# Kernel optimization log

Measured on AMD Instinct MI355X. Metric: run time of the kernel, lower is better.

## Reference

```python
import jax, jax.numpy as jnp
import numpy as np

B, S, H, D = 16, 2048, 768, 128
ATTR_MAX, ITEMS_MAX = 8, 32  # static equivalents of attr_type_ids.max() / item_position_ids max (data generated to hit these)


def setup_inputs() -> dict:
    key = jax.random.key(0)
    k1, k2, k3, k4 = jax.random.split(key, 4)
    return {
        "attention_mask": jnp.ones((B, S), dtype=jnp.int32),
        "hidden_states": jax.random.normal(k1, (B, S, H), dtype=jnp.float32),
        "attr_type_ids": jax.random.randint(k2, (B, S), 0, ATTR_MAX + 1),
        "item_position_ids": jax.random.randint(k3, (B, S), 0, ITEMS_MAX + 1),
        "W": jax.random.normal(k4, (H, D), dtype=jnp.float32) * (1.0 / np.sqrt(H)),
        "b": jnp.zeros((D,), dtype=jnp.float32),
    }


def reference(attention_mask, hidden_states, attr_type_ids, item_position_ids, W, b):
    # linear projection: [B,S,H] @ [H,D] -> [B,S,D]
    h = jnp.einsum('bsh,hd->bsd', hidden_states, W) + b
    Bn, Sn, Dn = h.shape

    # segmented mean over (attr_id, item_id) groups; attr/item id 0 (and >max, e.g. the 50 pad sentinel) are invalid
    valid = (attr_type_ids >= 1) & (attr_type_ids <= ATTR_MAX) & \
            (item_position_ids >= 1) & (item_position_ids <= ITEMS_MAX)
    batch_idx = jnp.arange(Bn)[:, None]
    seg = (batch_idx * ATTR_MAX + (attr_type_ids - 1)) * ITEMS_MAX + (item_position_ids - 1)
    nseg = Bn * ATTR_MAX * ITEMS_MAX
    seg = jnp.where(valid, seg, nseg)  # dump invalid tokens into extra segment
    flat_seg = seg.reshape(-1)

    sums = jax.ops.segment_sum(h.reshape(-1, Dn), flat_seg, num_segments=nseg + 1)[:nseg]
    counts = jax.ops.segment_sum(valid.reshape(-1).astype(h.dtype), flat_seg, num_segments=nseg + 1)[:nseg]

    sums = sums.reshape(Bn, ATTR_MAX, ITEMS_MAX, Dn)
    counts = counts.reshape(Bn, ATTR_MAX, ITEMS_MAX)
    empty = counts == 0
    pooled = sums / jnp.where(empty, jnp.ones_like(counts), counts)[..., None]
    return pooled, empty, h
```

## Files before the change

kernel.cpp:

```cpp
#include <hip/hip_runtime.h>
#include <hip/hip_bf16.h>

#define Bn 16
#define Sn 2048
#define Hn 768
#define Dn 128
#define AT 8
#define IT 32
#define NSEG (Bn*AT*IT)

typedef __attribute__((ext_vector_type(4))) float f32x4;
typedef __attribute__((ext_vector_type(4))) int   i32x4;
typedef __attribute__((ext_vector_type(8))) short bf16x8;
typedef __attribute__((ext_vector_type(4))) short s16x4;

__device__ __forceinline__ unsigned short f2bf(float f){
  union { float f; unsigned u; } v; v.f = f;
  unsigned r = v.u + 0x7FFFu + ((v.u >> 16) & 1u);
  return (unsigned short)(r >> 16);
}

__global__ __launch_bounds__(256) void k_prep(const float* __restrict__ W,
                                              unsigned short* __restrict__ Wt){
  __shared__ float sT[64][65];
  const int tid = threadIdx.x;
  const int k0 = (blockIdx.x % 12) * 64;
  const int d0 = (blockIdx.x / 12) * 64;
  const int rr = tid >> 4;
  const int cg = tid & 15;

  #pragma unroll
  for (int p = 0; p < 4; ++p){
    int k = rr + p*16;
    f32x4 v = *(const f32x4*)&W[(size_t)(k0 + k)*Dn + d0 + cg*4];
    sT[k][cg*4+0] = v[0]; sT[k][cg*4+1] = v[1];
    sT[k][cg*4+2] = v[2]; sT[k][cg*4+3] = v[3];
  }
  __syncthreads();
  #pragma unroll
  for (int p = 0; p < 4; ++p){
    int d = rr + p*16;
    s16x4 t;
    #pragma unroll
    for (int j = 0; j < 4; ++j) t[j] = (short)f2bf(sT[cg*4+j][d]);
    *(s16x4*)&Wt[(size_t)(d0 + d)*Hn + k0 + cg*4] = t;
  }
}

__global__ __launch_bounds__(256) void k_gemm(const float* __restrict__ X,
        const unsigned short* __restrict__ Wt, const float* __restrict__ bias,
        float* __restrict__ Hout){
  __shared__ unsigned char sA[2][64*128];
  __shared__ unsigned char sB[2][128*128];
  const int tid  = threadIdx.x;
  const int lane = tid & 63;
  const int wave = tid >> 6;
  const int m0 = blockIdx.x * 64;

  const int ar = tid >> 2, akq = tid & 3;
  const int bc = tid >> 1, bkh = tid & 1;
  const float*          Ap = X  + (size_t)(m0 + ar)*Hn + akq*4;
  const unsigned short* Bp = Wt + (size_t)bc*Hn + bkh*32;

  int aw[4], bw[4];
  #pragma unroll
  for (int c=0;c<4;c++) aw[c] = ar*128 + ((akq*8 + c*32) ^ ((ar&7)<<4));
  #pragma unroll
  for (int c=0;c<4;c++) bw[c] = bc*128 + ((bkh*64 + c*16) ^ ((bc&7)<<4));

  int abase[4], aswz[4];
  #pragma unroll
  for (int mi=0;mi<4;mi++){
    int row = mi*16 + (lane&15);
    abase[mi] = row*128; aswz[mi] = (row&7)<<4;
  }
  int bbase[2], bswz[2];
  #pragma unroll
  for (int ni=0;ni<2;ni++){
    int col = wave*32 + ni*16 + (lane&15);
    bbase[ni] = col*128; bswz[ni] = (col&7)<<4;
  }
  const int kblk = (lane>>4)*16;

  f32x4 acc[4][2];
  #pragma unroll
  for (int mi=0;mi<4;mi++)
    #pragma unroll
    for (int ni=0;ni<2;ni++) acc[mi][ni] = (f32x4){0.f,0.f,0.f,0.f};

  f32x4 av[4]; i32x4 bv[4];
  #pragma unroll
  for (int c=0;c<4;c++) av[c] = *(const f32x4*)(Ap + c*16);
  #pragma unroll
  for (int c=0;c<4;c++) bv[c] = *(const i32x4*)(Bp + c*8);
  #pragma unroll
  for (int c=0;c<4;c++){
    s16x4 t;
    t[0]=(short)f2bf(av[c][0]); t[1]=(short)f2bf(av[c][1]);
    t[2]=(short)f2bf(av[c][2]); t[3]=(short)f2bf(av[c][3]);
    *(s16x4*)&sA[0][aw[c]] = t;
  }
  #pragma unroll
  for (int c=0;c<4;c++) *(i32x4*)&sB[0][bw[c]] = bv[c];
  __syncthreads();

  int cur = 0;
  for (int step=0; step<12; ++step){
    if (step < 11){
      #pragma unroll
      for (int c=0;c<4;c++) av[c] = *(const f32x4*)(Ap + (step+1)*64 + c*16);
      #pragma unroll
      for (int c=0;c<4;c++) bv[c] = *(const i32x4*)(Bp + (step+1)*64 + c*8);
    }
    #pragma unroll
    for (int ks=0; ks<2; ++ks){
      bf16x8 af[4], bfv[2];
      #pragma unroll
      for (int mi=0;mi<4;mi++)
        af[mi] = *(const bf16x8*)&sA[cur][abase[mi] + ((ks*64 + kblk) ^ aswz[mi])];
      #pragma unroll
      for (int ni=0;ni<2;ni++)
        bfv[ni] = *(const bf16x8*)&sB[cur][bbase[ni] + ((ks*64 + kblk) ^ bswz[ni])];
      #pragma unroll
      for (int mi=0;mi<4;mi++)
        #pragma unroll
        for (int ni=0;ni<2;ni++)
          acc[mi][ni] = __builtin_amdgcn_mfma_f32_16x16x32_bf16(af[mi], bfv[ni], acc[mi][ni], 0, 0, 0);
    }
    if (step < 11){
      #pragma unroll
      for (int c=0;c<4;c++){
        s16x4 t;
        t[0]=(short)f2bf(av[c][0]); t[1]=(short)f2bf(av[c][1]);
        t[2]=(short)f2bf(av[c][2]); t[3]=(short)f2bf(av[c][3]);
        *(s16x4*)&sA[cur^1][aw[c]] = t;
      }
      #pragma unroll
      for (int c=0;c<4;c++) *(i32x4*)&sB[cur^1][bw[c]] = bv[c];
    }
    __syncthreads();
    cur ^= 1;
  }

  #pragma unroll
  for (int ni=0;ni<2;ni++){
    int col = wave*32 + ni*16 + (lane&15);
    float bb = bias[col];
    #pragma unroll
    for (int mi=0;mi<4;mi++){
      int row0 = m0 + mi*16 + (lane>>4)*4;
      #pragma unroll
      for (int r=0;r<4;r++)
        Hout[(size_t)(row0 + r)*Dn + col] = acc[mi][ni][r] + bb;
    }
  }
}

__global__ __launch_bounds__(256) void k_scan(const int* __restrict__ attr,
        const int* __restrict__ item, const float* __restrict__ Hsrc,
        float* __restrict__ pooled, float* __restrict__ empty){
  __shared__ float ssum[4][IT][64];
  __shared__ int   slist[4][512];
  __shared__ int   scnt[IT];

  const int wg  = blockIdx.x;
  const int dh  = wg & 1;
  const int a   = (wg >> 1) & 7;
  const int b   = wg >> 4;
  const int tid = threadIdx.x;
  const int wv  = tid >> 6;
  const int lane = tid & 63;

  #pragma unroll
  for (int i = 0; i < IT; ++i) ssum[wv][i][lane] = 0.f;
  if (tid < IT) scnt[tid] = 0;

  const int tok0 = wv * 512;
  const int gbase = b * Sn;
  int nm = 0;
  #pragma unroll
  for (int g = 0; g < 8; ++g){
    int tok = tok0 + g*64 + lane;
    int avv = attr[gbase + tok], ivv = item[gbase + tok];
    bool m = (avv == a+1) && (ivv >= 1) && (ivv <= IT);
    unsigned long long mask = __ballot(m);
    int pos = nm + __popcll(mask & ((1ull << lane) - 1ull));
    if (m) slist[wv][pos] = ((ivv-1) << 16) | tok;
    nm += __popcll(mask);
  }
  __syncthreads();

  for (int e = lane; e < nm; e += 64) atomicAdd(&scnt[slist[wv][e] >> 16], 1);

  const float* hb = Hsrc + (size_t)b*Sn*Dn + dh*64 + lane;
  int e = 0;
  for (; e + 8 <= nm; e += 8){
    int idx[8]; float v[8];
    #pragma unroll
    for (int j=0;j<8;j++) idx[j] = slist[wv][e+j];
    #pragma unroll
    for (int j=0;j<8;j++) v[j] = hb[(size_t)(idx[j] & 0xffff)*Dn];
    #pragma unroll
    for (int j=0;j<8;j++) ssum[wv][idx[j]>>16][lane] += v[j];
  }
  for (; e < nm; ++e){
    int idx = slist[wv][e];
    ssum[wv][idx>>16][lane] += hb[(size_t)(idx & 0xffff)*Dn];
  }
  __syncthreads();

  float* outp = pooled + (size_t)(b*AT + a)*IT*Dn + dh*64;
  for (int o = tid; o < IT*64; o += 256){
    int i = o >> 6, d = o & 63;
    float s = ssum[0][i][d] + ssum[1][i][d] + ssum[2][i][d] + ssum[3][i][d];
    int cnt = scnt[i];
    outp[i*Dn + d] = s / (float)(cnt > 0 ? cnt : 1);
  }
  if (dh == 0 && tid < IT)
    empty[(b*AT + a)*IT + tid] = (scnt[tid] == 0) ? 1.f : 0.f;
}

extern "C" void kernel_launch(void* const* d_in, const int* in_sizes, int n_in,
                              void* d_out, int out_size, void* d_ws, size_t ws_size,
                              hipStream_t stream) {
  const float* hidden = (const float*)d_in[1];
  const int*   attr   = (const int*)  d_in[2];
  const int*   item   = (const int*)  d_in[3];
  const float* W      = (const float*)d_in[4];
  const float* bias   = (const float*)d_in[5];

  float* pooled = (float*)d_out;
  float* empty  = pooled + (size_t)NSEG*Dn;
  float* Hout   = empty  + NSEG;

  unsigned short* Wt = (unsigned short*)d_ws;

  k_prep<<<24, 256, 0, stream>>>(W, Wt);
  k_gemm<<<(Bn*Sn)/64, 256, 0, stream>>>(hidden, Wt, bias, Hout);
  k_scan<<<Bn*AT*2, 256, 0, stream>>>(attr, item, Hout, pooled, empty);
}
```

Measured before the change: 39.43 us.

## Deepen GEMM global prefetch to two stages with register double-buffering

The GEMM main loop now keeps two sets of register buffers, so global loads are issued two K-steps ahead. The LDS store of the previously loaded tile is moved before the MFMA block, and the loop is fully unrolled with a compile-time buffer index. The float-to-bf16 conversion also switches to the HIP intrinsic. This aims to hide more global memory latency in a bandwidth-bound GEMM, at the cost of higher register pressure that may reduce occupancy.

```diff
diff --git a/kernel.cpp b/kernel.cpp
--- a/kernel.cpp
+++ b/kernel.cpp
@@ -15,9 +15,8 @@
 typedef __attribute__((ext_vector_type(4))) short s16x4;
 
 __device__ __forceinline__ unsigned short f2bf(float f){
-  union { float f; unsigned u; } v; v.f = f;
-  unsigned r = v.u + 0x7FFFu + ((v.u >> 16) & 1u);
-  return (unsigned short)(r >> 16);
+  __hip_bfloat16 h = __float2bfloat16(f);
+  return *reinterpret_cast<unsigned short*>(&h);
 }
 
 __global__ __launch_bounds__(256) void k_prep(const float* __restrict__ W,
@@ -88,29 +87,51 @@
     #pragma unroll
     for (int ni=0;ni<2;ni++) acc[mi][ni] = (f32x4){0.f,0.f,0.f,0.f};
 
-  f32x4 av[4]; i32x4 bv[4];
-  #pragma unroll
-  for (int c=0;c<4;c++) av[c] = *(const f32x4*)(Ap + c*16);
-  #pragma unroll
-  for (int c=0;c<4;c++) bv[c] = *(const i32x4*)(Bp + c*8);
+  f32x4 av[2][4]; i32x4 bv[2][4];
+
+  #pragma unroll
+  for (int c=0;c<4;c++) av[0][c] = *(const f32x4*)(Ap + c*16);
+  #pragma unroll
+  for (int c=0;c<4;c++) bv[0][c] = *(const i32x4*)(Bp + c*8);
   #pragma unroll
   for (int c=0;c<4;c++){
     s16x4 t;
-    t[0]=(short)f2bf(av[c][0]); t[1]=(short)f2bf(av[c][1]);
-    t[2]=(short)f2bf(av[c][2]); t[3]=(short)f2bf(av[c][3]);
+    t[0]=(short)f2bf(av[0][c][0]); t[1]=(short)f2bf(av[0][c][1]);
+    t[2]=(short)f2bf(av[0][c][2]); t[3]=(short)f2bf(av[0][c][3]);
     *(s16x4*)&sA[0][aw[c]] = t;
   }
   #pragma unroll
-  for (int c=0;c<4;c++) *(i32x4*)&sB[0][bw[c]] = bv[c];
-  __syncthreads();
-
-  int cur = 0;
+  for (int c=0;c<4;c++) *(i32x4*)&sB[0][bw[c]] = bv[0][c];
+  #pragma unroll
+  for (int c=0;c<4;c++) av[1][c] = *(const f32x4*)(Ap + 64 + c*16);
+  #pragma unroll
+  for (int c=0;c<4;c++) bv[1][c] = *(const i32x4*)(Bp + 64 + c*8);
+  #pragma unroll
+  for (int c=0;c<4;c++) av[0][c] = *(const f32x4*)(Ap + 128 + c*16);
+  #pragma unroll
+  for (int c=0;c<4;c++) bv[0][c] = *(const i32x4*)(Bp + 128 + c*8);
+  __syncthreads();
+
+  #pragma unroll
   for (int step=0; step<12; ++step){
+    const int cur = step & 1;
+    const int p   = (step+1) & 1;
     if (step < 11){
       #pragma unroll
-      for (int c=0;c<4;c++) av[c] = *(const f32x4*)(Ap + (step+1)*64 + c*16);
-      #pragma unroll
-      for (int c=0;c<4;c++) bv[c] = *(const i32x4*)(Bp + (step+1)*64 + c*8);
+      for (int c=0;c<4;c++){
+        s16x4 t;
+        t[0]=(short)f2bf(av[p][c][0]); t[1]=(short)f2bf(av[p][c][1]);
+        t[2]=(short)f2bf(av[p][c][2]); t[3]=(short)f2bf(av[p][c][3]);
+        *(s16x4*)&sA[cur^1][aw[c]] = t;
+      }
+      #pragma unroll
+      for (int c=0;c<4;c++) *(i32x4*)&sB[cur^1][bw[c]] = bv[p][c];
+    }
+    if (step < 9){
+      #pragma unroll
+      for (int c=0;c<4;c++) av[p][c] = *(const f32x4*)(Ap + (step+3)*64 + c*16);
+      #pragma unroll
+      for (int c=0;c<4;c++) bv[p][c] = *(const i32x4*)(Bp + (step+3)*64 + c*8);
     }
     #pragma unroll
     for (int ks=0; ks<2; ++ks){
@@ -127,19 +148,7 @@
         for (int ni=0;ni<2;ni++)
           acc[mi][ni] = __builtin_amdgcn_mfma_f32_16x16x32_bf16(af[mi], bfv[ni], acc[mi][ni], 0, 0, 0);
     }
-    if (step < 11){
-      #pragma unroll
-      for (int c=0;c<4;c++){
-        s16x4 t;
-        t[0]=(short)f2bf(av[c][0]); t[1]=(short)f2bf(av[c][1]);
-        t[2]=(short)f2bf(av[c][2]); t[3]=(short)f2bf(av[c][3]);
-        *(s16x4*)&sA[cur^1][aw[c]] = t;
-      }
-      #pragma unroll
-      for (int c=0;c<4;c++) *(i32x4*)&sB[cur^1][bw[c]] = bv[c];
-    }
     __syncthreads();
-    cur ^= 1;
   }
 
   #pragma unroll
```

Result: no change. 39.84 us (+1.0%).

## Fuse GEMM and segmented-mean scan into one kernel with per-batch completion flags

Applied to the files above, without the earlier changes.

Merges the projection GEMM and the segment-pooling scan into a single kernel. The first 256 tiles go on to do the scan work after their GEMM tile, reusing the shared memory through a union. Each scan block waits on a per-batch atomic counter until all 32 GEMM tiles for that batch have written their H rows. The change removes one kernel launch and the gap between launches, and lets the scan for early batches overlap with GEMM tiles still running. In exchange it relies on inter-block spin-waiting, which could deadlock if the waiting blocks occupy the GPU before the producing tiles are scheduled, and it swaps the manual bf16 rounding for the library conversion.

```diff
diff --git a/kernel.cpp b/kernel.cpp
--- a/kernel.cpp
+++ b/kernel.cpp
@@ -15,15 +15,17 @@
 typedef __attribute__((ext_vector_type(4))) short s16x4;
 
 __device__ __forceinline__ unsigned short f2bf(float f){
-  union { float f; unsigned u; } v; v.f = f;
-  unsigned r = v.u + 0x7FFFu + ((v.u >> 16) & 1u);
-  return (unsigned short)(r >> 16);
+  __hip_bfloat16 h = __float2bfloat16(f);
+  return *reinterpret_cast<unsigned short*>(&h);
 }
 
 __global__ __launch_bounds__(256) void k_prep(const float* __restrict__ W,
-                                              unsigned short* __restrict__ Wt){
+                                              unsigned short* __restrict__ Wt,
+                                              int* __restrict__ flags){
   __shared__ float sT[64][65];
   const int tid = threadIdx.x;
+  if (blockIdx.x == 0 && tid < Bn)
+    __hip_atomic_store(&flags[tid], 0, __ATOMIC_RELAXED, __HIP_MEMORY_SCOPE_AGENT);
   const int k0 = (blockIdx.x % 12) * 64;
   const int d0 = (blockIdx.x / 12) * 64;
   const int rr = tid >> 4;
@@ -47,133 +49,137 @@
   }
 }
 
-__global__ __launch_bounds__(256) void k_gemm(const float* __restrict__ X,
+__global__ __launch_bounds__(256) void k_fused(const float* __restrict__ X,
         const unsigned short* __restrict__ Wt, const float* __restrict__ bias,
-        float* __restrict__ Hout){
-  __shared__ unsigned char sA[2][64*128];
-  __shared__ unsigned char sB[2][128*128];
+        const int* __restrict__ attr, const int* __restrict__ item,
+        float* __restrict__ Hout, float* __restrict__ pooled,
+        float* __restrict__ empty, int* __restrict__ flags){
+  __shared__ union {
+    struct { unsigned char a[2][64*128]; unsigned char b[2][128*128]; } g;
+    struct { float ssum[4][IT][64]; int slist[4][512]; int scnt[IT]; } s;
+  } u;
+
   const int tid  = threadIdx.x;
   const int lane = tid & 63;
   const int wave = tid >> 6;
-  const int m0 = blockIdx.x * 64;
-
-  const int ar = tid >> 2, akq = tid & 3;
-  const int bc = tid >> 1, bkh = tid & 1;
-  const float*          Ap = X  + (size_t)(m0 + ar)*Hn + akq*4;
-  const unsigned short* Bp = Wt + (size_t)bc*Hn + bkh*32;
-
-  int aw[4], bw[4];
-  #pragma unroll
-  for (int c=0;c<4;c++) aw[c] = ar*128 + ((akq*8 + c*32) ^ ((ar&7)<<4));
-  #pragma unroll
-  for (int c=0;c<4;c++) bw[c] = bc*128 + ((bkh*64 + c*16) ^ ((bc&7)<<4));
-
-  int abase[4], aswz[4];
-  #pragma unroll
-  for (int mi=0;mi<4;mi++){
-    int row = mi*16 + (lane&15);
-    abase[mi] = row*128; aswz[mi] = (row&7)<<4;
-  }
-  int bbase[2], bswz[2];
-  #pragma unroll
-  for (int ni=0;ni<2;ni++){
-    int col = wave*32 + ni*16 + (lane&15);
-    bbase[ni] = col*128; bswz[ni] = (col&7)<<4;
-  }
-  const int kblk = (lane>>4)*16;
-
-  f32x4 acc[4][2];
-  #pragma unroll
-  for (int mi=0;mi<4;mi++)
-    #pragma unroll
-    for (int ni=0;ni<2;ni++) acc[mi][ni] = (f32x4){0.f,0.f,0.f,0.f};
-
-  f32x4 av[4]; i32x4 bv[4];
-  #pragma unroll
-  for (int c=0;c<4;c++) av[c] = *(const f32x4*)(Ap + c*16);
-  #pragma unroll
-  for (int c=0;c<4;c++) bv[c] = *(const i32x4*)(Bp + c*8);
-  #pragma unroll
-  for (int c=0;c<4;c++){
-    s16x4 t;
-    t[0]=(short)f2bf(av[c][0]); t[1]=(short)f2bf(av[c][1]);
-    t[2]=(short)f2bf(av[c][2]); t[3]=(short)f2bf(av[c][3]);
-    *(s16x4*)&sA[0][aw[c]] = t;
-  }
-  #pragma unroll
-  for (int c=0;c<4;c++) *(i32x4*)&sB[0][bw[c]] = bv[c];
-  __syncthreads();
-
-  int cur = 0;
-  for (int step=0; step<12; ++step){
-    if (step < 11){
+  const int tile = blockIdx.x;
+  const int m0 = tile * 64;
+
+  {
+    const int ar = tid >> 2, akq = tid & 3;
+    const int bc = tid >> 1, bkh = tid & 1;
+    const float*          Ap = X  + (size_t)(m0 + ar)*Hn + akq*4;
+    const unsigned short* Bp = Wt + (size_t)bc*Hn + bkh*32;
+
+    int aw[4], bw[4];
+    #pragma unroll
+    for (int c=0;c<4;c++) aw[c] = ar*128 + ((akq*8 + c*32) ^ ((ar&7)<<4));
+    #pragma unroll
+    for (int c=0;c<4;c++) bw[c] = bc*128 + ((bkh*64 + c*16) ^ ((bc&7)<<4));
+
+    int abase[4], aswz[4];
+    #pragma unroll
+    for (int mi=0;mi<4;mi++){
+      int row = mi*16 + (lane&15);
+      abase[mi] = row*128; aswz[mi] = (row&7)<<4;
+    }
+    int bbase[2], bswz[2];
+    #pragma unroll
+    for (int ni=0;ni<2;ni++){
+      int col = wave*32 + ni*16 + (lane&15);
+      bbase[ni] = col*128; bswz[ni] = (col&7)<<4;
+    }
+    const int kblk = (lane>>4)*16;
+
+    f32x4 acc[4][2];
+    #pragma unroll
+    for (int mi=0;mi<4;mi++)
       #pragma unroll
-      for (int c=0;c<4;c++) av[c] = *(const f32x4*)(Ap + (step+1)*64 + c*16);
+      for (int ni=0;ni<2;ni++) acc[mi][ni] = (f32x4){0.f,0.f,0.f,0.f};
+
+    f32x4 av[4]; i32x4 bv[4];
+    #pragma unroll
+    for (int c=0;c<4;c++) av[c] = *(const f32x4*)(Ap + c*16);
+    #pragma unroll
+    for (int c=0;c<4;c++) bv[c] = *(const i32x4*)(Bp + c*8);
+    #pragma unroll
+    for (int c=0;c<4;c++){
+      s16x4 t;
+      t[0]=(short)f2bf(av[c][0]); t[1]=(short)f2bf(av[c][1]);
+      t[2]=(short)f2bf(av[c][2]); t[3]=(short)f2bf(av[c][3]);
+      *(s16x4*)&u.g.a[0][aw[c]] = t;
+    }
+    #pragma unroll
+    for (int c=0;c<4;c++) *(i32x4*)&u.g.b[0][bw[c]] = bv[c];
+    __syncthreads();
+
+    int cur = 0;
+    for (int step=0; step<12; ++step){
+      if (step < 11){
+        #pragma unroll
+        for (int c=0;c<4;c++) av[c] = *(const f32x4*)(Ap + (step+1)*64 + c*16);
+        #pragma unroll
+        for (int c=0;c<4;c++) bv[c] = *(const i32x4*)(Bp + (step+1)*64 + c*8);
+      }
       #pragma unroll
-      for (int c=0;c<4;c++) bv[c] = *(const i32x4*)(Bp + (step+1)*64 + c*8);
-    }
-    #pragma unroll
-    for (int ks=0; ks<2; ++ks){
-      bf16x8 af[4], bfv[2];
+      for (int ks=0; ks<2; ++ks){
+        bf16x8 af[4], bfv[2];
+        #pragma unroll
+        for (int mi=0;mi<4;mi++)
+          af[mi] = *(const bf16x8*)&u.g.a[cur][abase[mi] + ((ks*64 + kblk) ^ aswz[mi])];
+        #pragma unroll
+        for (int ni=0;ni<2;ni++)
+          bfv[ni] = *(const bf16x8*)&u.g.b[cur][bbase[ni] + ((ks*64 + kblk) ^ bswz[ni])];
+        #pragma unroll
+        for (int mi=0;mi<4;mi++)
+          #pragma unroll
+          for (int ni=0;ni<2;ni++)
+            acc[mi][ni] = __builtin_amdgcn_mfma_f32_16x16x32_bf16(af[mi], bfv[ni], acc[mi][ni], 0, 0, 0);
+      }
+      if (step < 11){
+        #pragma unroll
+        for (int c=0;c<4;c++){
+          s16x4 t;
+          t[0]=(short)f2bf(av[c][0]); t[1]=(short)f2bf(av[c][1]);
+          t[2]=(short)f2bf(av[c][2]); t[3]=(short)f2bf(av[c][3]);
+          *(s16x4*)&u.g.a[cur^1][aw[c]] = t;
+        }
+        #pragma unroll
+        for (int c=0;c<4;c++) *(i32x4*)&u.g.b[cur^1][bw[c]] = bv[c];
+      }
+      __syncthreads();
+      cur ^= 1;
+    }
+
+    #pragma unroll
+    for (int ni=0;ni<2;ni++){
+      int col = wave*32 + ni*16 + (lane&15);
+      float bb = bias[col];
       #pragma unroll
-      for (int mi=0;mi<4;mi++)
-        af[mi] = *(const bf16x8*)&sA[cur][abase[mi] + ((ks*64 + kblk) ^ aswz[mi])];
-      #pragma unroll
-      for (int ni=0;ni<2;ni++)
-        bfv[ni] = *(const bf16x8*)&sB[cur][bbase[ni] + ((ks*64 + kblk) ^ bswz[ni])];
-      #pragma unroll
-      for (int mi=0;mi<4;mi++)
-        #pragma unroll
-        for (int ni=0;ni<2;ni++)
-          acc[mi][ni] = __builtin_amdgcn_mfma_f32_16x16x32_bf16(af[mi], bfv[ni], acc[mi][ni], 0, 0, 0);
-    }
-    if (step < 11){
-      #pragma unroll
-      for (int c=0;c<4;c++){
-        s16x4 t;
-        t[0]=(short)f2bf(av[c][0]); t[1]=(short)f2bf(av[c][1]);
-        t[2]=(short)f2bf(av[c][2]); t[3]=(short)f2bf(av[c][3]);
-        *(s16x4*)&sA[cur^1][aw[c]] = t;
-      }
-      #pragma unroll
-      for (int c=0;c<4;c++) *(i32x4*)&sB[cur^1][bw[c]] = bv[c];
-    }
-    __syncthreads();
-    cur ^= 1;
-  }
-
-  #pragma unroll
-  for (int ni=0;ni<2;ni++){
-    int col = wave*32 + ni*16 + (lane&15);
-    float bb = bias[col];
-    #pragma unroll
-    for (int mi=0;mi<4;mi++){
-      int row0 = m0 + mi*16 + (lane>>4)*4;
-      #pragma unroll
-      for (int r=0;r<4;r++)
-        Hout[(size_t)(row0 + r)*Dn + col] = acc[mi][ni][r] + bb;
-    }
-  }
-}
-
-__global__ __launch_bounds__(256) void k_scan(const int* __restrict__ attr,
-        const int* __restrict__ item, const float* __restrict__ Hsrc,
-        float* __restrict__ pooled, float* __restrict__ empty){
-  __shared__ float ssum[4][IT][64];
-  __shared__ int   slist[4][512];
-  __shared__ int   scnt[IT];
-
-  const int wg  = blockIdx.x;
+      for (int mi=0;mi<4;mi++){
+        int row0 = m0 + mi*16 + (lane>>4)*4;
+        #pragma unroll
+        for (int r=0;r<4;r++)
+          Hout[(size_t)(row0 + r)*Dn + col] = acc[mi][ni][r] + bb;
+      }
+    }
+  }
+
+  __syncthreads();
+  if (tid == 0)
+    __hip_atomic_fetch_add(&flags[tile >> 5], 1, __ATOMIC_RELEASE, __HIP_MEMORY_SCOPE_AGENT);
+
+  if (tile >= Bn*AT*2) return;
+
+  const int wg  = tile;
   const int dh  = wg & 1;
   const int a   = (wg >> 1) & 7;
   const int b   = wg >> 4;
-  const int tid = threadIdx.x;
-  const int wv  = tid >> 6;
-  const int lane = tid & 63;
-
-  #pragma unroll
-  for (int i = 0; i < IT; ++i) ssum[wv][i][lane] = 0.f;
-  if (tid < IT) scnt[tid] = 0;
+  const int wv  = wave;
+
+  #pragma unroll
+  for (int i = 0; i < IT; ++i) u.s.ssum[wv][i][lane] = 0.f;
+  if (tid < IT) u.s.scnt[tid] = 0;
 
   const int tok0 = wv * 512;
   const int gbase = b * Sn;
@@ -185,39 +191,46 @@
     bool m = (avv == a+1) && (ivv >= 1) && (ivv <= IT);
     unsigned long long mask = __ballot(m);
     int pos = nm + __popcll(mask & ((1ull << lane) - 1ull));
-    if (m) slist[wv][pos] = ((ivv-1) << 16) | tok;
+    if (m) u.s.slist[wv][pos] = ((ivv-1) << 16) | tok;
     nm += __popcll(mask);
   }
   __syncthreads();
 
-  for (int e = lane; e < nm; e += 64) atomicAdd(&scnt[slist[wv][e] >> 16], 1);
-
-  const float* hb = Hsrc + (size_t)b*Sn*Dn + dh*64 + lane;
+  for (int e = lane; e < nm; e += 64) atomicAdd(&u.s.scnt[u.s.slist[wv][e] >> 16], 1);
+
+  if (tid == 0){
+    while (__hip_atomic_load(&flags[b], __ATOMIC_ACQUIRE, __HIP_MEMORY_SCOPE_AGENT) < 32)
+      __builtin_amdgcn_s_sleep(2);
+  }
+  __syncthreads();
+  (void)__hip_atomic_load(&flags[b], __ATOMIC_ACQUIRE, __HIP_MEMORY_SCOPE_AGENT);
+
+  const float* hb = Hout + (size_t)b*Sn*Dn + dh*64 + lane;
   int e = 0;
   for (; e + 8 <= nm; e += 8){
     int idx[8]; float v[8];
     #pragma unroll
-    for (int j=0;j<8;j++) idx[j] = slist[wv][e+j];
+    for (int j=0;j<8;j++) idx[j] = u.s.slist[wv][e+j];
     #pragma unroll
     for (int j=0;j<8;j++) v[j] = hb[(size_t)(idx[j] & 0xffff)*Dn];
     #pragma unroll
-    for (int j=0;j<8;j++) ssum[wv][idx[j]>>16][lane] += v[j];
+    for (int j=0;j<8;j++) u.s.ssum[wv][idx[j]>>16][lane] += v[j];
   }
   for (; e < nm; ++e){
-    int idx = slist[wv][e];
-    ssum[wv][idx>>16][lane] += hb[(size_t)(idx & 0xffff)*Dn];
+    int idx = u.s.slist[wv][e];
+    u.s.ssum[wv][idx>>16][lane] += hb[(size_t)(idx & 0xffff)*Dn];
   }
   __syncthreads();
 
   float* outp = pooled + (size_t)(b*AT + a)*IT*Dn + dh*64;
   for (int o = tid; o < IT*64; o += 256){
     int i = o >> 6, d = o & 63;
-    float s = ssum[0][i][d] + ssum[1][i][d] + ssum[2][i][d] + ssum[3][i][d];
-    int cnt = scnt[i];
+    float s = u.s.ssum[0][i][d] + u.s.ssum[1][i][d] + u.s.ssum[2][i][d] + u.s.ssum[3][i][d];
+    int cnt = u.s.scnt[i];
     outp[i*Dn + d] = s / (float)(cnt > 0 ? cnt : 1);
   }
   if (dh == 0 && tid < IT)
-    empty[(b*AT + a)*IT + tid] = (scnt[tid] == 0) ? 1.f : 0.f;
+    empty[(b*AT + a)*IT + tid] = (u.s.scnt[tid] == 0) ? 1.f : 0.f;
 }
 
 extern "C" void kernel_launch(void* const* d_in, const int* in_sizes, int n_in,
@@ -234,8 +247,9 @@
   float* Hout   = empty  + NSEG;
 
   unsigned short* Wt = (unsigned short*)d_ws;
-
-  k_prep<<<24, 256, 0, stream>>>(W, Wt);
-  k_gemm<<<(Bn*Sn)/64, 256, 0, stream>>>(hidden, Wt, bias, Hout);
-  k_scan<<<Bn*AT*2, 256, 0, stream>>>(attr, item, Hout, pooled, empty);
-}
+  int* flags = (int*)((char*)d_ws + 196608);
+
+  k_prep<<<24, 256, 0, stream>>>(W, Wt, flags);
+  k_fused<<<(Bn*Sn)/64, 256, 0, stream>>>(hidden, Wt, bias, attr, item,
+                                          Hout, pooled, empty, flags);
+}
```

New measurement: 91.28 us. 2.32x slower.

## Load B fragments directly from global and deepen A prefetch pipeline

Applied to the files above, without the earlier changes.

The GEMM kernel stops staging the transposed bf16 weight tile in LDS and instead loads each wave's B fragments straight from global memory into registers, double-buffered across K steps. The A tile now uses a two-deep register prefetch, converting the next step's data into LDS before issuing loads for the step after, with raw s_barrier and sched_barrier in place of __syncthreads. The float-to-bf16 conversion also switches to the HIP intrinsic. This is meant to cut LDS traffic and capacity and to hide global load latency better, at the cost of more registers and redundant global reads of W across waves and blocks.

```diff
diff --git a/kernel.cpp b/kernel.cpp
--- a/kernel.cpp
+++ b/kernel.cpp
@@ -15,9 +15,8 @@
 typedef __attribute__((ext_vector_type(4))) short s16x4;
 
 __device__ __forceinline__ unsigned short f2bf(float f){
-  union { float f; unsigned u; } v; v.f = f;
-  unsigned r = v.u + 0x7FFFu + ((v.u >> 16) & 1u);
-  return (unsigned short)(r >> 16);
+  __hip_bfloat16 h = __float2bfloat16(f);
+  return *reinterpret_cast<unsigned short*>(&h);
 }
 
 __global__ __launch_bounds__(256) void k_prep(const float* __restrict__ W,
@@ -51,36 +50,34 @@
         const unsigned short* __restrict__ Wt, const float* __restrict__ bias,
         float* __restrict__ Hout){
   __shared__ unsigned char sA[2][64*128];
-  __shared__ unsigned char sB[2][128*128];
   const int tid  = threadIdx.x;
   const int lane = tid & 63;
   const int wave = tid >> 6;
-  const int m0 = blockIdx.x * 64;
-
-  const int ar = tid >> 2, akq = tid & 3;
-  const int bc = tid >> 1, bkh = tid & 1;
-  const float*          Ap = X  + (size_t)(m0 + ar)*Hn + akq*4;
-  const unsigned short* Bp = Wt + (size_t)bc*Hn + bkh*32;
-
-  int aw[4], bw[4];
-  #pragma unroll
-  for (int c=0;c<4;c++) aw[c] = ar*128 + ((akq*8 + c*32) ^ ((ar&7)<<4));
-  #pragma unroll
-  for (int c=0;c<4;c++) bw[c] = bc*128 + ((bkh*64 + c*16) ^ ((bc&7)<<4));
+  const int m0   = blockIdx.x * 64;
+  const int r16  = lane & 15, kg = lane >> 4;
+
+  const int r0 = tid >> 4;
+  const int kq = tid & 15;
+  const float* Ap = X + (size_t)(m0 + r0)*Hn + kq*4;
+  int awoff[4];
+  #pragma unroll
+  for (int i=0;i<4;i++){
+    int row = r0 + i*16;
+    awoff[i] = row*128 + ((kq*8) ^ ((row&7)<<4));
+  }
+
+  const unsigned short* Bp[2];
+  #pragma unroll
+  for (int ni=0;ni<2;ni++)
+    Bp[ni] = Wt + (size_t)(wave*32 + ni*16 + r16)*Hn + kg*8;
 
   int abase[4], aswz[4];
   #pragma unroll
   for (int mi=0;mi<4;mi++){
-    int row = mi*16 + (lane&15);
+    int row = mi*16 + r16;
     abase[mi] = row*128; aswz[mi] = (row&7)<<4;
   }
-  int bbase[2], bswz[2];
-  #pragma unroll
-  for (int ni=0;ni<2;ni++){
-    int col = wave*32 + ni*16 + (lane&15);
-    bbase[ni] = col*128; bswz[ni] = (col&7)<<4;
-  }
-  const int kblk = (lane>>4)*16;
+  const int kblk = kg*16;
 
   f32x4 acc[4][2];
   #pragma unroll
@@ -88,67 +85,79 @@
     #pragma unroll
     for (int ni=0;ni<2;ni++) acc[mi][ni] = (f32x4){0.f,0.f,0.f,0.f};
 
-  f32x4 av[4]; i32x4 bv[4];
-  #pragma unroll
-  for (int c=0;c<4;c++) av[c] = *(const f32x4*)(Ap + c*16);
-  #pragma unroll
-  for (int c=0;c<4;c++) bv[c] = *(const i32x4*)(Bp + c*8);
-  #pragma unroll
-  for (int c=0;c<4;c++){
+  f32x4  a4[2][4];
+  bf16x8 bv[2][4];
+
+  #pragma unroll
+  for (int i=0;i<4;i++) a4[0][i] = *(const f32x4*)(Ap + (size_t)i*16*Hn);
+  #pragma unroll
+  for (int i=0;i<4;i++) a4[1][i] = *(const f32x4*)(Ap + (size_t)i*16*Hn + 64);
+  #pragma unroll
+  for (int ks=0;ks<2;ks++)
+    #pragma unroll
+    for (int ni=0;ni<2;ni++)
+      bv[0][ks*2+ni] = *(const bf16x8*)(Bp[ni] + ks*32);
+  #pragma unroll
+  for (int i=0;i<4;i++){
     s16x4 t;
-    t[0]=(short)f2bf(av[c][0]); t[1]=(short)f2bf(av[c][1]);
-    t[2]=(short)f2bf(av[c][2]); t[3]=(short)f2bf(av[c][3]);
-    *(s16x4*)&sA[0][aw[c]] = t;
-  }
-  #pragma unroll
-  for (int c=0;c<4;c++) *(i32x4*)&sB[0][bw[c]] = bv[c];
-  __syncthreads();
-
-  int cur = 0;
-  for (int step=0; step<12; ++step){
-    if (step < 11){
-      #pragma unroll
-      for (int c=0;c<4;c++) av[c] = *(const f32x4*)(Ap + (step+1)*64 + c*16);
-      #pragma unroll
-      for (int c=0;c<4;c++) bv[c] = *(const i32x4*)(Bp + (step+1)*64 + c*8);
-    }
-    #pragma unroll
-    for (int ks=0; ks<2; ++ks){
-      bf16x8 af[4], bfv[2];
+    t[0]=(short)f2bf(a4[0][i][0]); t[1]=(short)f2bf(a4[0][i][1]);
+    t[2]=(short)f2bf(a4[0][i][2]); t[3]=(short)f2bf(a4[0][i][3]);
+    *(s16x4*)&sA[0][awoff[i]] = t;
+  }
+  asm volatile("s_waitcnt lgkmcnt(0)" ::: "memory");
+  __builtin_amdgcn_s_barrier();
+  __builtin_amdgcn_sched_barrier(0);
+
+  #pragma unroll
+  for (int s=0; s<12; ++s){
+    const int pb = (s+1)&1;
+    if (s < 11){
+      #pragma unroll
+      for (int i=0;i<4;i++){
+        s16x4 t;
+        t[0]=(short)f2bf(a4[pb][i][0]); t[1]=(short)f2bf(a4[pb][i][1]);
+        t[2]=(short)f2bf(a4[pb][i][2]); t[3]=(short)f2bf(a4[pb][i][3]);
+        *(s16x4*)&sA[pb][awoff[i]] = t;
+      }
+    }
+    if (s < 10){
+      #pragma unroll
+      for (int i=0;i<4;i++)
+        a4[s&1][i] = *(const f32x4*)(Ap + (size_t)i*16*Hn + (s+2)*64);
+    }
+    if (s < 11){
+      #pragma unroll
+      for (int ks=0;ks<2;ks++)
+        #pragma unroll
+        for (int ni=0;ni<2;ni++)
+          bv[pb][ks*2+ni] = *(const bf16x8*)(Bp[ni] + (s+1)*64 + ks*32);
+    }
+    #pragma unroll
+    for (int ks=0;ks<2;ks++){
+      bf16x8 af[4];
       #pragma unroll
       for (int mi=0;mi<4;mi++)
-        af[mi] = *(const bf16x8*)&sA[cur][abase[mi] + ((ks*64 + kblk) ^ aswz[mi])];
-      #pragma unroll
-      for (int ni=0;ni<2;ni++)
-        bfv[ni] = *(const bf16x8*)&sB[cur][bbase[ni] + ((ks*64 + kblk) ^ bswz[ni])];
+        af[mi] = *(const bf16x8*)&sA[s&1][abase[mi] + ((ks*64 + kblk) ^ aswz[mi])];
       #pragma unroll
       for (int mi=0;mi<4;mi++)
         #pragma unroll
         for (int ni=0;ni<2;ni++)
-          acc[mi][ni] = __builtin_amdgcn_mfma_f32_16x16x32_bf16(af[mi], bfv[ni], acc[mi][ni], 0, 0, 0);
-    }
-    if (step < 11){
-      #pragma unroll
-      for (int c=0;c<4;c++){
-        s16x4 t;
-        t[0]=(short)f2bf(av[c][0]); t[1]=(short)f2bf(av[c][1]);
-        t[2]=(short)f2bf(av[c][2]); t[3]=(short)f2bf(av[c][3]);
-        *(s16x4*)&sA[cur^1][aw[c]] = t;
-      }
-      #pragma unroll
-      for (int c=0;c<4;c++) *(i32x4*)&sB[cur^1][bw[c]] = bv[c];
-    }
-    __syncthreads();
-    cur ^= 1;
+          acc[mi][ni] = __builtin_amdgcn_mfma_f32_16x16x32_bf16(af[mi], bv[s&1][ks*2+ni], acc[mi][ni], 0, 0, 0);
+    }
+    if (s < 11){
+      asm volatile("s_waitcnt lgkmcnt(0)" ::: "memory");
+      __builtin_amdgcn_s_barrier();
+      __builtin_amdgcn_sched_barrier(0);
+    }
   }
 
   #pragma unroll
   for (int ni=0;ni<2;ni++){
-    int col = wave*32 + ni*16 + (lane&15);
+    int col = wave*32 + ni*16 + r16;
     float bb = bias[col];
     #pragma unroll
     for (int mi=0;mi<4;mi++){
-      int row0 = m0 + mi*16 + (lane>>4)*4;
+      int row0 = m0 + mi*16 + kg*4;
       #pragma unroll
       for (int r=0;r<4;r++)
         Hout[(size_t)(row0 + r)*Dn + col] = acc[mi][ni][r] + bb;
```

Measured after the change: 40.73 us. +3.3%, slower.
